# Optimization experiments

Hardware: AMD Instinct MI355X
Metric: run time of the kernel (lower is better)

Reference implementation:

```python
import jax, jax.numpy as jnp
import numpy as np

N = 33           # n_nodes (fixed by lstm1 input_size = 512*33)
T = 1024         # seq_length
E_RAND = 64      # random directed edges
E = E_RAND + N   # plus self-loops (PyG GATv2Conv add_self_loops=True)
H1, C1 = 8, 64   # gat1: heads, out_channels
C2 = 512         # gat2: out_channels, 1 head
D_IN, D_EDGE = 2, 3
HID1, HID2, N_CLASSES = 128, 64, 4


def _p(k, shape):
    return jax.random.normal(k, shape, dtype=jnp.float32) * 0.05


def setup_inputs() -> dict:
    key = jax.random.key(0)
    ks = jax.random.split(key, 30)
    src = jax.random.randint(ks[0], (E_RAND,), 0, N)
    dst = jax.random.randint(ks[1], (E_RAND,), 0, N)
    loop = jnp.arange(N)
    edge_index = jnp.stack([jnp.concatenate([src, loop]),
                            jnp.concatenate([dst, loop])]).astype(jnp.int32)
    return {
        'x': jax.random.normal(ks[2], (T, N, D_IN), dtype=jnp.float32),
        'edge_index': edge_index,
        'edge_attr': jax.random.normal(ks[3], (E, D_EDGE), dtype=jnp.float32),
        'g1_wl': _p(ks[4], (D_IN, H1 * C1)),
        'g1_wr': _p(ks[5], (D_IN, H1 * C1)),
        'g1_we': _p(ks[6], (D_EDGE, H1 * C1)),
        'g1_att': _p(ks[7], (H1, C1)),
        'g1_b': _p(ks[8], (H1 * C1,)),
        'g2_wl': _p(ks[9], (H1 * C1, C2)),
        'g2_wr': _p(ks[10], (H1 * C1, C2)),
        'g2_we': _p(ks[11], (D_EDGE, C2)),
        'g2_att': _p(ks[12], (1, C2)),
        'g2_b': _p(ks[13], (C2,)),
        'l1_wih': _p(ks[14], (4 * HID1, N * C2)),
        'l1_whh': _p(ks[15], (4 * HID1, HID1)),
        'l1_bih': _p(ks[16], (4 * HID1,)),
        'l1_bhh': _p(ks[17], (4 * HID1,)),
        'l2_wih': _p(ks[18], (4 * HID2, HID1)),
        'l2_whh': _p(ks[19], (4 * HID2, HID2)),
        'l2_bih': _p(ks[20], (4 * HID2,)),
        'l2_bhh': _p(ks[21], (4 * HID2,)),
        'fc_w': _p(ks[22], (N_CLASSES, HID2)),
        'fc_b': _p(ks[23], (N_CLASSES,)),
    }


def _gatv2(x, src, dst, edge_attr, wl, wr, we, att, bias, heads, ch):
    # GATv2 with edge features, vectorized over the time axis.
    # x: [T,N,Din] -> out [T,N,heads*ch]
    Tt, Nn, _ = x.shape
    xl = (x @ wl).reshape(Tt, Nn, heads, ch)   # source projection
    xr = (x @ wr).reshape(Tt, Nn, heads, ch)   # target projection
    ep = (edge_attr @ we).reshape(-1, heads, ch)
    msg = xl[:, src]                                        # [T,E,H,C]
    e = jax.nn.leaky_relu(msg + xr[:, dst] + ep[None], 0.2)  # GATv2 score input
    logits = jnp.einsum('tehc,hc->eth', e, att)             # edge-first [E,T,H]
    m = jax.ops.segment_max(logits, dst, num_segments=Nn)
    m = jnp.where(jnp.isneginf(m), 0.0, m)
    ex = jnp.exp(logits - m[dst])
    denom = jax.ops.segment_sum(ex, dst, num_segments=Nn)
    alpha = ex / (denom[dst] + 1e-16)                       # [E,T,H]
    out = jax.ops.segment_sum(alpha[..., None] * jnp.swapaxes(msg, 0, 1),
                              dst, num_segments=Nn)          # [N,T,H,C]
    return jnp.swapaxes(out, 0, 1).reshape(Tt, Nn, heads * ch) + bias


def _lstm(xs, wih, whh, bih, bhh):
    # PyTorch LSTM, batch=1, gate order i,f,g,o. xs: [T,D] -> [T,H]
    hd = whh.shape[1]
    def step(carry, xt):
        h, c = carry
        z = xt @ wih.T + h @ whh.T + bih + bhh
        i, f, g, o = jnp.split(z, 4)
        c = jax.nn.sigmoid(f) * c + jax.nn.sigmoid(i) * jnp.tanh(g)
        h = jax.nn.sigmoid(o) * jnp.tanh(c)
        return (h, c), h
    h0 = jnp.zeros((hd,), xs.dtype)
    _, hs = jax.lax.scan(step, (h0, h0), xs)
    return hs


def _forward(edge_index, x, edge_attr, g1_wl, g1_wr, g1_we, g1_att, g1_b,
             g2_wl, g2_wr, g2_we, g2_att, g2_b,
             l1_wih, l1_whh, l1_bih, l1_bhh,
             l2_wih, l2_whh, l2_bih, l2_bhh, fc_w, fc_b):
    src, dst = edge_index[0], edge_index[1]
    h = jax.nn.elu(_gatv2(x, src, dst, edge_attr, g1_wl, g1_wr, g1_we, g1_att, g1_b, H1, C1))
    h = jax.nn.elu(_gatv2(h, src, dst, edge_attr, g2_wl, g2_wr, g2_we, g2_att, g2_b, 1, C2))
    # torch: stack [T,N,512] -> permute(1,0,2) -> reshape(1, T, N*512)
    seq = jnp.transpose(h, (1, 0, 2)).reshape(T, N * C2)
    hs = _lstm(seq, l1_wih, l1_whh, l1_bih, l1_bhh)
    hs = _lstm(hs, l2_wih, l2_whh, l2_bih, l2_bhh)
    return (hs[-1] @ fc_w.T + fc_b)[None, :]  # [1, n_classes]


def reference(x, edge_index, edge_attr, g1_wl, g1_wr, g1_we, g1_att, g1_b,
              g2_wl, g2_wr, g2_we, g2_att, g2_b,
              l1_wih, l1_whh, l1_bih, l1_bhh,
              l2_wih, l2_whh, l2_bih, l2_bhh, fc_w, fc_b):
    return _forward(edge_index, x, edge_attr, g1_wl, g1_wr, g1_we, g1_att, g1_b,
                    g2_wl, g2_wr, g2_we, g2_att, g2_b,
                    l1_wih, l1_whh, l1_bih, l1_bhh,
                    l2_wih, l2_whh, l2_bih, l2_bhh, fc_w, fc_b)
```

## Files before the change

### kernel.cpp

```cpp
#include <hip/hip_runtime.h>

typedef unsigned short u16;
typedef unsigned int   u32;
typedef __attribute__((ext_vector_type(8))) short  short8;
typedef __attribute__((ext_vector_type(8))) unsigned short ushort8;
typedef __attribute__((ext_vector_type(4))) float  f32x4;

#define NT 1024
#define NN 33
#define NE 97

__device__ __forceinline__ float b2f(u16 u){ return __uint_as_float(((u32)u)<<16); }
__device__ __forceinline__ u16 f2b(float f){
    u32 x = __float_as_uint(f);
    return (u16)((x + 0x7fffu + ((x>>16)&1u)) >> 16);
}
__device__ __forceinline__ float sigm(float x){ return 1.f/(1.f+__expf(-x)); }
__device__ __forceinline__ float tanh_(float x){ float e=__expf(2.f*x); return 1.f - 2.f/(e+1.f); }

__global__ void detect_kernel(const u32* g1_wl_raw, int* flag){
    if (threadIdx.x==0 && blockIdx.x==0){
        int hits=0;
        for (int k=0;k<256;k++){
            u32 w = g1_wl_raw[k];
            u32 e = (w>>7)&0xffu;
            if (e>=96u && e<=126u) hits++;
        }
        *flag = (hits>=160) ? 0 : 1;
    }
}

struct ConvArgs { const void* src[22]; int n[22]; int off[22]; };
__global__ void convert_kernel(ConvArgs a, const int* flag, u16* blob){
    bool isf32 = (*flag)!=0;
    int stride = gridDim.x*blockDim.x;
    for (int s=0;s<22;s++){
        int n=a.n[s]; const void* sp=a.src[s]; u16* dp=blob+a.off[s];
        for (int i=blockIdx.x*blockDim.x+threadIdx.x; i<n; i+=stride)
            dp[i] = isf32 ? f2b(((const float*)sp)[i]) : ((const u16*)sp)[i];
    }
}

#define CX      0
#define CEA     67584
#define CG1WL   67880
#define CG1WR   68904
#define CG1WE   69928
#define CG1ATT  71464
#define CG1B    71976
#define CG2WL   72488
#define CG2WR   334632
#define CG2WE   596776
#define CG2ATT  598312
#define CG2B    598824
#define CL1WIH  599336
#define CL1WHH  9250088
#define CL1BIH  9315624
#define CL1BHH  9316136
#define CL2WIH  9316648
#define CL2WHH  9349416
#define CL2BIH  9365800
#define CL2BHH  9366056
#define CFCW    9366312
#define CFCB    9366568

__global__ void setup_kernel(const int* ei, const u16* ea,
                             const u16* g1_we, const u16* g2_we,
                             int* csr, float* ep1, float* ep2)
{
    int tid = threadIdx.x;
    if (tid == 0) {
        int cnt[NN]; for (int n=0;n<NN;n++) cnt[n]=0;
        for (int e=0;e<NE;e++) cnt[ei[NE+e]]++;
        int off=0;
        for (int n=0;n<NN;n++){ csr[n]=off; off+=cnt[n]; }
        csr[NN]=off;
        int pos[NN]; for (int n=0;n<NN;n++) pos[n]=csr[n];
        for (int e=0;e<NE;e++){ int d=ei[NE+e]; csr[34+pos[d]]=e; pos[d]++; }
        for (int e=0;e<NE;e++){ csr[131+e]=ei[e]; csr[228+e]=ei[NE+e]; }
    }
    for (int i=tid; i<NE*512; i+=blockDim.x) {
        int e = i>>9, hc = i&511;
        float a0=b2f(ea[e*3]), a1=b2f(ea[e*3+1]), a2=b2f(ea[e*3+2]);
        ep1[i] = a0*b2f(g1_we[hc]) + a1*b2f(g1_we[512+hc]) + a2*b2f(g1_we[1024+hc]);
        ep2[i] = a0*b2f(g2_we[hc]) + a1*b2f(g2_we[512+hc]) + a2*b2f(g2_we[1024+hc]);
    }
}

__global__ void wlrt_kernel(const u16* g2_wl, const u16* g2_wr, u16* wlrt)
{
    int i = blockIdx.x*256 + threadIdx.x;
    int k = i>>9, c = i&511;
    wlrt[c*512 + k]        = g2_wl[i];
    wlrt[(c+512)*512 + k]  = g2_wr[i];
}

__global__ __launch_bounds__(256) void gat1_kernel(
    const u16* x, const u16* g1_wl, const u16* g1_wr, const u16* g1_att,
    const u16* g1_b, const float* ep1, const int* csr, u16* h1)
{
    __shared__ float wl[2][512], wr[2][512], att[512], bias[512];
    __shared__ float xt[2*NN];
    __shared__ float logits[NE*8];
    __shared__ float mmax[NN*8], den[NN*8];
    __shared__ int s_off[NN+1], s_eid[NE], s_src[NE], s_dst[NE];
    int t = blockIdx.x, tid = threadIdx.x;

    for (int i=tid;i<512;i+=256){
        wl[0][i]=b2f(g1_wl[i]);      wl[1][i]=b2f(g1_wl[512+i]);
        wr[0][i]=b2f(g1_wr[i]);      wr[1][i]=b2f(g1_wr[512+i]);
        att[i]=b2f(g1_att[i]);       bias[i]=b2f(g1_b[i]);
    }
    for (int i=tid;i<2*NN;i+=256) xt[i]=b2f(x[t*(2*NN)+i]);
    if (tid<NN+1) s_off[tid]=csr[tid];
    for (int i=tid;i<NE;i+=256){ s_eid[i]=csr[34+i]; s_src[i]=csr[131+i]; s_dst[i]=csr[228+i]; }
    __syncthreads();

    for (int i=tid; i<NE*8; i+=256) {
        int e=i>>3, h=i&7;
        int s=s_src[e], d=s_dst[e];
        float xs0=xt[s*2], xs1=xt[s*2+1], xd0=xt[d*2], xd1=xt[d*2+1];
        const float* epp = ep1 + e*512 + h*64;
        float acc=0.f;
        #pragma unroll 8
        for (int c=0;c<64;c++){
            int hc=h*64+c;
            float v = xs0*wl[0][hc] + xs1*wl[1][hc]
                    + xd0*wr[0][hc] + xd1*wr[1][hc] + epp[c];
            v = v>0.f ? v : 0.2f*v;
            acc += att[hc]*v;
        }
        logits[i]=acc;
    }
    __syncthreads();
    for (int i=tid; i<NN*8; i+=256) {
        int n=i>>3, h=i&7;
        float m=-1e30f;
        for (int p=s_off[n]; p<s_off[n+1]; ++p){ float v=logits[s_eid[p]*8+h]; m=v>m?v:m; }
        float s=0.f;
        for (int p=s_off[n]; p<s_off[n+1]; ++p) s += __expf(logits[s_eid[p]*8+h]-m);
        mmax[i]=m; den[i]=s+1e-16f;
    }
    __syncthreads();
    for (int i=tid; i<NE*8; i+=256) {
        int h=i&7, d=s_dst[i>>3];
        logits[i] = __expf(logits[i]-mmax[d*8+h]) / den[d*8+h];
    }
    __syncthreads();
    for (int i=tid; i<NN*512; i+=256) {
        int n=i>>9, hc=i&511, h=hc>>6;
        float acc=0.f;
        for (int p=s_off[n]; p<s_off[n+1]; ++p){
            int e=s_eid[p]; int s=s_src[e];
            float xlv = xt[s*2]*wl[0][hc] + xt[s*2+1]*wl[1][hc];
            acc += logits[e*8+h]*xlv;
        }
        acc += bias[hc];
        acc = acc>0.f ? acc : __expf(acc)-1.f;
        h1[(size_t)(t*NN+n)*512 + hc] = f2b(acc);
    }
}

__global__ __launch_bounds__(256) void gemm_nt(
    const u16* __restrict__ A, const u16* __restrict__ B, void* Cout,
    int M, int N, int K, int kChunk, int mode)
{
    __shared__ u16 lds_a[128*40];
    __shared__ u16 lds_b[128*40];
    const int nt = blockIdx.x, mt = blockIdx.y, kc = blockIdx.z;
    const int tid = threadIdx.x;
    const int wave = tid>>6, lane = tid&63;
    const int wm = (wave&1)*64, wn = (wave>>1)*64;
    const int l15 = lane&15, quad = lane>>4;
    const int srow = tid>>2, scol = (tid&3)*8;

    const u16* Ab = A + (size_t)mt*128*K;
    const u16* Bb = B + (size_t)nt*128*K;
    const int k0beg = kc*kChunk, k0end = k0beg + kChunk;

    f32x4 acc[4][4] = {};
    for (int k0 = k0beg; k0 < k0end; k0 += 32) {
        #pragma unroll
        for (int r = 0; r < 2; ++r) {
            int row = srow + r*64;
            *(ushort8*)&lds_a[row*40 + scol] = *(const ushort8*)&Ab[(size_t)row*K + k0 + scol];
            *(ushort8*)&lds_b[row*40 + scol] = *(const ushort8*)&Bb[(size_t)row*K + k0 + scol];
        }
        __syncthreads();
        short8 af[4], bfr[4];
        #pragma unroll
        for (int i=0;i<4;i++) af[i]  = *(const short8*)&lds_a[(wm + i*16 + l15)*40 + quad*8];
        #pragma unroll
        for (int j=0;j<4;j++) bfr[j] = *(const short8*)&lds_b[(wn + j*16 + l15)*40 + quad*8];
        #pragma unroll
        for (int i=0;i<4;i++)
            #pragma unroll
            for (int j=0;j<4;j++)
                acc[i][j] = __builtin_amdgcn_mfma_f32_16x16x32_bf16(af[i], bfr[j], acc[i][j], 0,0,0);
        __syncthreads();
    }
    if (mode == 0) {
        u16* Cb = (u16*)Cout;
        #pragma unroll
        for (int i=0;i<4;i++)
            #pragma unroll
            for (int j=0;j<4;j++)
                #pragma unroll
                for (int r=0;r<4;r++){
                    int row = mt*128 + wm + i*16 + quad*4 + r;
                    int col = nt*128 + wn + j*16 + l15;
                    Cb[(size_t)row*N + col] = f2b(acc[i][j][r]);
                }
    } else {
        float* Cb = (float*)Cout + (size_t)kc*M*N;
        #pragma unroll
        for (int i=0;i<4;i++)
            #pragma unroll
            for (int j=0;j<4;j++)
                #pragma unroll
                for (int r=0;r<4;r++){
                    int row = mt*128 + wm + i*16 + quad*4 + r;
                    int col = nt*128 + wn + j*16 + l15;
                    Cb[(size_t)row*N + col] = acc[i][j][r];
                }
    }
}

__global__ void reduce8_kernel(const float* part, float* out)
{
    int i = blockIdx.x*256 + threadIdx.x;
    float s=0.f;
    #pragma unroll
    for (int k=0;k<8;k++) s += part[(size_t)k*524288 + i];
    out[i]=s;
}

__global__ __launch_bounds__(256) void gat2_kernel(
    const u16* C, const u16* g2_att, const u16* g2_b, const float* ep2,
    const int* csr, u16* h2)
{
    __shared__ u16 xl[NN*512];
    __shared__ float att[512], bias[512];
    __shared__ float part[NE*8];
    __shared__ float logit[NE], alpha[NE], mm[NN], dd[NN];
    __shared__ int s_off[NN+1], s_eid[NE], s_src[NE], s_dst[NE];
    int t = blockIdx.x, tid = threadIdx.x;

    for (int i=tid;i<512;i+=256){ att[i]=b2f(g2_att[i]); bias[i]=b2f(g2_b[i]); }
    if (tid<NN+1) s_off[tid]=csr[tid];
    for (int i=tid;i<NE;i+=256){ s_eid[i]=csr[34+i]; s_src[i]=csr[131+i]; s_dst[i]=csr[228+i]; }
    for (int i=tid; i<NN*64; i+=256){
        int n=i>>6, q=i&63;
        *(ushort8*)&xl[n*512+q*8] = *(const ushort8*)&C[(size_t)(t*NN+n)*1024 + q*8];
    }
    __syncthreads();

    for (int i=tid; i<NE*8; i+=256){
        int e=i>>3, q=i&7;
        int s=s_src[e], d=s_dst[e];
        const u16* xrp = C + (size_t)(t*NN+d)*1024 + 512 + q*64;
        const float* epp = ep2 + e*512 + q*64;
        const u16* xlp = xl + s*512 + q*64;
        float acc=0.f;
        #pragma unroll 8
        for (int c=0;c<64;c++){
            float v = b2f(xlp[c]) + b2f(xrp[c]) + epp[c];
            v = v>0.f ? v : 0.2f*v;
            acc += att[q*64+c]*v;
        }
        part[i]=acc;
    }
    __syncthreads();
    for (int i=tid;i<NE;i+=256){
        float s=0.f;
        #pragma unroll
        for (int q=0;q<8;q++) s+=part[i*8+q];
        logit[i]=s;
    }
    __syncthreads();
    for (int i=tid;i<NN;i+=256){
        float m=-1e30f;
        for (int p=s_off[i];p<s_off[i+1];++p){ float v=logit[s_eid[p]]; m=v>m?v:m; }
        float s=0.f;
        for (int p=s_off[i];p<s_off[i+1];++p) s+=__expf(logit[s_eid[p]]-m);
        mm[i]=m; dd[i]=s+1e-16f;
    }
    __syncthreads();
    for (int i=tid;i<NE;i+=256) alpha[i]=__expf(logit[i]-mm[s_dst[i]])/dd[s_dst[i]];
    __syncthreads();
    for (int i=tid;i<NN*512;i+=256){
        int n=i>>9, c=i&511;
        float acc=0.f;
        for (int p=s_off[n];p<s_off[n+1];++p){ int e=s_eid[p]; acc += alpha[e]*b2f(xl[s_src[e]*512+c]); }
        acc += bias[c];
        acc = acc>0.f ? acc : __expf(acc)-1.f;
        h2[(size_t)n*524288 + (size_t)t*512 + c] = f2b(acc);
    }
}

__global__ __launch_bounds__(512) void lstm_fused_kernel(
    const float* __restrict__ pre1,
    const u16* __restrict__ whh1, const u16* b1ih, const u16* b1hh,
    const u16* __restrict__ w2ih, const u16* __restrict__ w2hh,
    const u16* b2ih, const u16* b2hh,
    const u16* fc_w, const u16* fc_b, const int* flag, void* outv)
{
    __shared__ __align__(16) float pre_c[32*512];
    __shared__ __align__(16) u16 hb1[128];
    __shared__ __align__(16) u16 hb2[64];
    __shared__ __align__(16) float z_lds[768];
    __shared__ float hf[64];
    const int tid = threadIdx.x;
    const int wave = tid>>6, lane = tid&63;
    const int l15 = lane&15, quad = lane>>4;
    const bool keep = (l15==0);
    const short8 zer = {0,0,0,0,0,0,0,0};
    const f32x4 fz = {0.f,0.f,0.f,0.f};
    const float4* p4g = (const float4*)pre1;
    float4* c4 = (float4*)pre_c;

    if (tid<128) hb1[tid]=0;
    if (wave==7) hb2[lane]=0;

    if (wave < 4) {
        short8 af[8][4];
        #pragma unroll
        for (int i=0;i<8;i++)
            #pragma unroll
            for (int c=0;c<4;c++)
                af[i][c] = *(const short8*)&whh1[(size_t)(wave*128 + i*16 + l15)*128 + c*32 + quad*8];
        float bz0=0,bz1=0,bz2=0,bz3=0, c1=0.f;
        if (tid<128){
            bz0 = b2f(b1ih[tid])     + b2f(b1hh[tid]);
            bz1 = b2f(b1ih[128+tid]) + b2f(b1hh[128+tid]);
            bz2 = b2f(b1ih[256+tid]) + b2f(b1hh[256+tid]);
            bz3 = b2f(b1ih[384+tid]) + b2f(b1hh[384+tid]);
        }
        __syncthreads();
        for (int k=0;k<=1024;k++){
            if (k<1024 && (k&31)==0){
                #pragma unroll
                for (int j=0;j<8;j++) c4[j*512+tid] = p4g[(size_t)k*128 + j*512 + tid];
                __syncthreads();
            }
            short8 bf[4];
            #pragma unroll
            for (int c=0;c<4;c++){
                short8 v = *(const short8*)&hb1[c*32 + quad*8];
                bf[c] = keep ? v : zer;
            }
            #pragma unroll
            for (int i=0;i<8;i++){
                f32x4 a = __builtin_amdgcn_mfma_f32_16x16x32_bf16(af[i][0], bf[0], fz, 0,0,0);
                a = __builtin_amdgcn_mfma_f32_16x16x32_bf16(af[i][1], bf[1], a, 0,0,0);
                a = __builtin_amdgcn_mfma_f32_16x16x32_bf16(af[i][2], bf[2], a, 0,0,0);
                a = __builtin_amdgcn_mfma_f32_16x16x32_bf16(af[i][3], bf[3], a, 0,0,0);
                if (keep) *(f32x4*)&z_lds[wave*128 + i*16 + quad*4] = a;
            }
            __syncthreads();
            if (k<1024 && tid<128){
                const float* pc = pre_c + (k&31)*512;
                float zi=z_lds[tid]    +pc[tid]    +bz0;
                float zf=z_lds[128+tid]+pc[128+tid]+bz1;
                float zg=z_lds[256+tid]+pc[256+tid]+bz2;
                float zo=z_lds[384+tid]+pc[384+tid]+bz3;
                c1 = sigm(zf)*c1 + sigm(zi)*tanh_(zg);
                float ho = sigm(zo)*tanh_(c1);
                hb1[tid] = f2b(ho);
            }
            __syncthreads();
        }
    } else {
        const int wv = wave-4;
        short8 af[4][6];
        #pragma unroll
        for (int i=0;i<4;i++){
            int r = wv*64 + i*16 + l15;
            #pragma unroll
            for (int c=0;c<4;c++)
                af[i][c] = *(const short8*)&w2ih[(size_t)r*128 + c*32 + quad*8];
            #pragma unroll
            for (int c=0;c<2;c++)
                af[i][4+c] = *(const short8*)&w2hh[(size_t)r*64 + c*32 + quad*8];
        }
        float bz0=0,bz1=0,bz2=0,bz3=0, c2=0.f;
        if (wave==7){
            bz0 = b2f(b2ih[lane])     + b2f(b2hh[lane]);
            bz1 = b2f(b2ih[64+lane])  + b2f(b2hh[64+lane]);
            bz2 = b2f(b2ih[128+lane]) + b2f(b2hh[128+lane]);
            bz3 = b2f(b2ih[192+lane]) + b2f(b2hh[192+lane]);
        }
        __syncthreads();
        for (int k=0;k<=1024;k++){
            if (k<1024 && (k&31)==0){
                #pragma unroll
                for (int j=0;j<8;j++) c4[j*512+tid] = p4g[(size_t)k*128 + j*512 + tid];
                __syncthreads();
            }
            short8 bf[6];
            #pragma unroll
            for (int c=0;c<4;c++){
                short8 v = *(const short8*)&hb1[c*32 + quad*8];
                bf[c] = keep ? v : zer;
            }
            #pragma unroll
            for (int c=0;c<2;c++){
                short8 v = *(const short8*)&hb2[c*32 + quad*8];
                bf[4+c] = keep ? v : zer;
            }
            #pragma unroll
            for (int i=0;i<4;i++){
                f32x4 a = __builtin_amdgcn_mfma_f32_16x16x32_bf16(af[i][0], bf[0], fz, 0,0,0);
                a = __builtin_amdgcn_mfma_f32_16x16x32_bf16(af[i][1], bf[1], a, 0,0,0);
                a = __builtin_amdgcn_mfma_f32_16x16x32_bf16(af[i][2], bf[2], a, 0,0,0);
                a = __builtin_amdgcn_mfma_f32_16x16x32_bf16(af[i][3], bf[3], a, 0,0,0);
                a = __builtin_amdgcn_mfma_f32_16x16x32_bf16(af[i][4], bf[4], a, 0,0,0);
                a = __builtin_amdgcn_mfma_f32_16x16x32_bf16(af[i][5], bf[5], a, 0,0,0);
                if (keep) *(f32x4*)&z_lds[512 + wv*64 + i*16 + quad*4] = a;
            }
            __syncthreads();
            if (k>=1 && wave==7){
                float zi=z_lds[512+lane]+bz0, zf=z_lds[576+lane]+bz1;
                float zg=z_lds[640+lane]+bz2, zo=z_lds[704+lane]+bz3;
                c2 = sigm(zf)*c2 + sigm(zi)*tanh_(zg);
                float ho = sigm(zo)*tanh_(c2);
                hb2[lane] = f2b(ho);
                hf[lane] = ho;
            }
            __syncthreads();
        }
    }
    __syncthreads();
    if (tid<4){
        float acc = b2f(fc_b[tid]);
        #pragma unroll
        for (int j=0;j<64;j++) acc += hf[j]*b2f(fc_w[tid*64+j]);
        if (*flag) ((float*)outv)[tid] = acc;
        else       ((u16*)outv)[tid]  = f2b(acc);
    }
}

extern "C" void kernel_launch(void* const* d_in, const int* in_sizes, int n_in,
                              void* d_out, int out_size, void* d_ws, size_t ws_size,
                              hipStream_t stream) {
    const int* ei = (const int*)d_in[1];
    char* ws = (char*)d_ws;

    const size_t o_blob = 0;
    const size_t o_h    = 18733184;
    const size_t o_C    = o_h    + 34603008;
    const size_t o_wlrt = o_C    + 69206016;
    const size_t o_ep1  = o_wlrt + 1048576;
    const size_t o_ep2  = o_ep1  + 198656;
    const size_t o_csr  = o_ep2  + 198656;
    const size_t o_pre1 = o_csr  + 2048;

    u16*   blob  = (u16*)(ws + o_blob);
    u16*   h_buf = (u16*)(ws + o_h);
    u16*   Cbuf  = (u16*)(ws + o_C);
    u16*   wlrt  = (u16*)(ws + o_wlrt);
    float* ep1   = (float*)(ws + o_ep1);
    float* ep2   = (float*)(ws + o_ep2);
    int*   csr   = (int*)(ws + o_csr);
    int*   flag  = csr + 400;
    float* pre1  = (float*)(ws + o_pre1);
    float* part  = (float*)(ws + o_C);

    detect_kernel<<<1,64,0,stream>>>((const u32*)d_in[3], flag);

    ConvArgs ca;
    const int blob_off[22] = {CX,CEA,CG1WL,CG1WR,CG1WE,CG1ATT,CG1B,
                              CG2WL,CG2WR,CG2WE,CG2ATT,CG2B,
                              CL1WIH,CL1WHH,CL1BIH,CL1BHH,
                              CL2WIH,CL2WHH,CL2BIH,CL2BHH,CFCW,CFCB};
    const int in_idx[22]   = {0,2,3,4,5,6,7,8,9,10,11,12,13,14,15,16,17,18,19,20,21,22};
    for (int s=0;s<22;s++){
        ca.src[s]=d_in[in_idx[s]]; ca.n[s]=in_sizes[in_idx[s]]; ca.off[s]=blob_off[s];
    }
    convert_kernel<<<2048,256,0,stream>>>(ca, flag, blob);

    setup_kernel<<<1,256,0,stream>>>(ei, blob+CEA, blob+CG1WE, blob+CG2WE, csr, ep1, ep2);
    wlrt_kernel<<<1024,256,0,stream>>>(blob+CG2WL, blob+CG2WR, wlrt);
    gat1_kernel<<<NT,256,0,stream>>>(blob+CX, blob+CG1WL, blob+CG1WR, blob+CG1ATT,
                                     blob+CG1B, ep1, csr, h_buf);
    gemm_nt<<<dim3(8,264,1),256,0,stream>>>(h_buf, wlrt, Cbuf, 33792, 1024, 512, 512, 0);
    gat2_kernel<<<NT,256,0,stream>>>(Cbuf, blob+CG2ATT, blob+CG2B, ep2, csr, h_buf);
    gemm_nt<<<dim3(4,8,8),256,0,stream>>>(h_buf, blob+CL1WIH, part, 1024, 512, 16896, 2112, 1);
    reduce8_kernel<<<2048,256,0,stream>>>(part, pre1);
    lstm_fused_kernel<<<1,512,0,stream>>>(pre1,
        blob+CL1WHH, blob+CL1BIH, blob+CL1BHH,
        blob+CL2WIH, blob+CL2WHH, blob+CL2BIH, blob+CL2BHH,
        blob+CFCW, blob+CFCB, flag, d_out);
}
```

Baseline: 1.574 ms.

## Interleave LSTM gate rows so MFMA lanes compute cell updates in registers

A new kernel permutes the recurrent and input weight rows so the four gates of each hidden unit are adjacent, and the reduce kernel writes the precomputed input projections in the same interleaved order. Each MFMA lane therefore holds all four gate pre-activations for its unit and applies the LSTM cell update directly from registers. This removes the z_lds round-trip and one barrier per timestep. The hidden state is double-buffered in LDS so reads of the previous step and writes of the current step do not conflict. The cost is an extra small permute kernel and more complex lane-to-unit indexing.

```diff
diff --git a/kernel.cpp b/kernel.cpp
--- a/kernel.cpp
+++ b/kernel.cpp
@@ -95,6 +95,25 @@
     wlrt[(c+512)*512 + k]  = g2_wr[i];
 }
 
+__global__ void permw_kernel(const u16* w1hh, const u16* w2ih, const u16* w2hh,
+                             u16* w1p, u16* w2ip, u16* w2hp)
+{
+    int i0 = blockIdx.x*256 + threadIdx.x;
+    int stride = gridDim.x*256;
+    for (int j=i0; j<65536; j+=stride){
+        int r=j>>7, k=j&127, u=r>>2, g=r&3;
+        w1p[j] = w1hh[(g*128+u)*128 + k];
+    }
+    for (int j=i0; j<32768; j+=stride){
+        int r=j>>7, k=j&127, u=r>>2, g=r&3;
+        w2ip[j] = w2ih[(g*64+u)*128 + k];
+    }
+    for (int j=i0; j<16384; j+=stride){
+        int r=j>>6, k=j&63, u=r>>2, g=r&3;
+        w2hp[j] = w2hh[(g*64+u)*64 + k];
+    }
+}
+
 __global__ __launch_bounds__(256) void gat1_kernel(
     const u16* x, const u16* g1_wl, const u16* g1_wr, const u16* g1_att,
     const u16* g1_b, const float* ep1, const int* csr, u16* h1)
@@ -232,7 +251,8 @@
     float s=0.f;
     #pragma unroll
     for (int k=0;k<8;k++) s += part[(size_t)k*524288 + i];
-    out[i]=s;
+    int t=i>>9, c=i&511;
+    out[t*512 + ((c&127)<<2) + (c>>7)] = s;
 }
 
 __global__ __launch_bounds__(256) void gat2_kernel(
@@ -299,28 +319,25 @@
 }
 
 __global__ __launch_bounds__(512) void lstm_fused_kernel(
-    const float* __restrict__ pre1,
-    const u16* __restrict__ whh1, const u16* b1ih, const u16* b1hh,
-    const u16* __restrict__ w2ih, const u16* __restrict__ w2hh,
+    const float* __restrict__ pre1p,
+    const u16* __restrict__ w1p, const u16* b1ih, const u16* b1hh,
+    const u16* __restrict__ w2ip, const u16* __restrict__ w2hp,
     const u16* b2ih, const u16* b2hh,
     const u16* fc_w, const u16* fc_b, const int* flag, void* outv)
 {
     __shared__ __align__(16) float pre_c[32*512];
-    __shared__ __align__(16) u16 hb1[128];
-    __shared__ __align__(16) u16 hb2[64];
-    __shared__ __align__(16) float z_lds[768];
+    __shared__ __align__(16) u16 hb1[2][128];
+    __shared__ __align__(16) u16 hb2[2][64];
     __shared__ float hf[64];
     const int tid = threadIdx.x;
     const int wave = tid>>6, lane = tid&63;
     const int l15 = lane&15, quad = lane>>4;
-    const bool keep = (l15==0);
-    const short8 zer = {0,0,0,0,0,0,0,0};
     const f32x4 fz = {0.f,0.f,0.f,0.f};
-    const float4* p4g = (const float4*)pre1;
+    const float4* p4g = (const float4*)pre1p;
     float4* c4 = (float4*)pre_c;
 
-    if (tid<128) hb1[tid]=0;
-    if (wave==7) hb2[lane]=0;
+    if (tid<128) hb1[1][tid]=0;
+    if (tid<64)  hb2[1][tid]=0;
 
     if (wave < 4) {
         short8 af[8][4];
@@ -328,45 +345,49 @@
         for (int i=0;i<8;i++)
             #pragma unroll
             for (int c=0;c<4;c++)
-                af[i][c] = *(const short8*)&whh1[(size_t)(wave*128 + i*16 + l15)*128 + c*32 + quad*8];
-        float bz0=0,bz1=0,bz2=0,bz3=0, c1=0.f;
-        if (tid<128){
-            bz0 = b2f(b1ih[tid])     + b2f(b1hh[tid]);
-            bz1 = b2f(b1ih[128+tid]) + b2f(b1hh[128+tid]);
-            bz2 = b2f(b1ih[256+tid]) + b2f(b1hh[256+tid]);
-            bz3 = b2f(b1ih[384+tid]) + b2f(b1hh[384+tid]);
-        }
+                af[i][c] = *(const short8*)&w1p[(size_t)(wave*128 + i*16 + l15)*128 + c*32 + quad*8];
+        const int u = wave*32 + ((l15<8)?l15:0)*4 + quad;
+        const float bz0 = b2f(b1ih[u])     + b2f(b1hh[u]);
+        const float bz1 = b2f(b1ih[128+u]) + b2f(b1hh[128+u]);
+        const float bz2 = b2f(b1ih[256+u]) + b2f(b1hh[256+u]);
+        const float bz3 = b2f(b1ih[384+u]) + b2f(b1hh[384+u]);
+        float c1 = 0.f;
         __syncthreads();
-        for (int k=0;k<=1024;k++){
+        for (int k=0;k<1025;k++){
             if (k<1024 && (k&31)==0){
                 #pragma unroll
                 for (int j=0;j<8;j++) c4[j*512+tid] = p4g[(size_t)k*128 + j*512 + tid];
                 __syncthreads();
             }
-            short8 bf[4];
-            #pragma unroll
-            for (int c=0;c<4;c++){
-                short8 v = *(const short8*)&hb1[c*32 + quad*8];
-                bf[c] = keep ? v : zer;
-            }
-            #pragma unroll
-            for (int i=0;i<8;i++){
-                f32x4 a = __builtin_amdgcn_mfma_f32_16x16x32_bf16(af[i][0], bf[0], fz, 0,0,0);
-                a = __builtin_amdgcn_mfma_f32_16x16x32_bf16(af[i][1], bf[1], a, 0,0,0);
-                a = __builtin_amdgcn_mfma_f32_16x16x32_bf16(af[i][2], bf[2], a, 0,0,0);
-                a = __builtin_amdgcn_mfma_f32_16x16x32_bf16(af[i][3], bf[3], a, 0,0,0);
-                if (keep) *(f32x4*)&z_lds[wave*128 + i*16 + quad*4] = a;
-            }
-            __syncthreads();
-            if (k<1024 && tid<128){
-                const float* pc = pre_c + (k&31)*512;
-                float zi=z_lds[tid]    +pc[tid]    +bz0;
-                float zf=z_lds[128+tid]+pc[128+tid]+bz1;
-                float zg=z_lds[256+tid]+pc[256+tid]+bz2;
-                float zo=z_lds[384+tid]+pc[384+tid]+bz3;
-                c1 = sigm(zf)*c1 + sigm(zi)*tanh_(zg);
-                float ho = sigm(zo)*tanh_(c1);
-                hb1[tid] = f2b(ho);
+            if (k<1024){
+                float4 pf = {0.f,0.f,0.f,0.f};
+                if (l15<8) pf = *(const float4*)&pre_c[(k&31)*512 + wave*128 + l15*16 + quad*4];
+                const u16* hp = hb1[(k+1)&1];
+                short8 b0 = *(const short8*)&hp[quad*8];
+                short8 b1 = *(const short8*)&hp[32+quad*8];
+                short8 b2 = *(const short8*)&hp[64+quad*8];
+                short8 b3 = *(const short8*)&hp[96+quad*8];
+                f32x4 acc[8];
+                #pragma unroll
+                for (int i=0;i<8;i++){
+                    f32x4 a = __builtin_amdgcn_mfma_f32_16x16x32_bf16(af[i][0], b0, fz, 0,0,0);
+                    a = __builtin_amdgcn_mfma_f32_16x16x32_bf16(af[i][1], b1, a, 0,0,0);
+                    a = __builtin_amdgcn_mfma_f32_16x16x32_bf16(af[i][2], b2, a, 0,0,0);
+                    a = __builtin_amdgcn_mfma_f32_16x16x32_bf16(af[i][3], b3, a, 0,0,0);
+                    acc[i] = a;
+                }
+                f32x4 z = acc[0];
+                #pragma unroll
+                for (int i=1;i<8;i++) z = (l15==i) ? acc[i] : z;
+                if (l15<8){
+                    float zi = z[0]+pf.x+bz0;
+                    float zf = z[1]+pf.y+bz1;
+                    float zg = z[2]+pf.z+bz2;
+                    float zo = z[3]+pf.w+bz3;
+                    c1 = sigm(zf)*c1 + sigm(zi)*tanh_(zg);
+                    float ho = sigm(zo)*tanh_(c1);
+                    hb1[k&1][u] = f2b(ho);
+                }
             }
             __syncthreads();
         }
@@ -378,54 +399,57 @@
             int r = wv*64 + i*16 + l15;
             #pragma unroll
             for (int c=0;c<4;c++)
-                af[i][c] = *(const short8*)&w2ih[(size_t)r*128 + c*32 + quad*8];
+                af[i][c] = *(const short8*)&w2ip[(size_t)r*128 + c*32 + quad*8];
             #pragma unroll
             for (int c=0;c<2;c++)
-                af[i][4+c] = *(const short8*)&w2hh[(size_t)r*64 + c*32 + quad*8];
-        }
-        float bz0=0,bz1=0,bz2=0,bz3=0, c2=0.f;
-        if (wave==7){
-            bz0 = b2f(b2ih[lane])     + b2f(b2hh[lane]);
-            bz1 = b2f(b2ih[64+lane])  + b2f(b2hh[64+lane]);
-            bz2 = b2f(b2ih[128+lane]) + b2f(b2hh[128+lane]);
-            bz3 = b2f(b2ih[192+lane]) + b2f(b2hh[192+lane]);
-        }
+                af[i][4+c] = *(const short8*)&w2hp[(size_t)r*64 + c*32 + quad*8];
+        }
+        const int u2 = wv*16 + ((l15<4)?l15:0)*4 + quad;
+        const float bz0 = b2f(b2ih[u2])     + b2f(b2hh[u2]);
+        const float bz1 = b2f(b2ih[64+u2])  + b2f(b2hh[64+u2]);
+        const float bz2 = b2f(b2ih[128+u2]) + b2f(b2hh[128+u2]);
+        const float bz3 = b2f(b2ih[192+u2]) + b2f(b2hh[192+u2]);
+        float c2s = 0.f;
         __syncthreads();
-        for (int k=0;k<=1024;k++){
+        for (int k=0;k<1025;k++){
             if (k<1024 && (k&31)==0){
                 #pragma unroll
                 for (int j=0;j<8;j++) c4[j*512+tid] = p4g[(size_t)k*128 + j*512 + tid];
                 __syncthreads();
             }
-            short8 bf[6];
-            #pragma unroll
-            for (int c=0;c<4;c++){
-                short8 v = *(const short8*)&hb1[c*32 + quad*8];
-                bf[c] = keep ? v : zer;
-            }
-            #pragma unroll
-            for (int c=0;c<2;c++){
-                short8 v = *(const short8*)&hb2[c*32 + quad*8];
-                bf[4+c] = keep ? v : zer;
-            }
-            #pragma unroll
-            for (int i=0;i<4;i++){
-                f32x4 a = __builtin_amdgcn_mfma_f32_16x16x32_bf16(af[i][0], bf[0], fz, 0,0,0);
-                a = __builtin_amdgcn_mfma_f32_16x16x32_bf16(af[i][1], bf[1], a, 0,0,0);
-                a = __builtin_amdgcn_mfma_f32_16x16x32_bf16(af[i][2], bf[2], a, 0,0,0);
-                a = __builtin_amdgcn_mfma_f32_16x16x32_bf16(af[i][3], bf[3], a, 0,0,0);
-                a = __builtin_amdgcn_mfma_f32_16x16x32_bf16(af[i][4], bf[4], a, 0,0,0);
-                a = __builtin_amdgcn_mfma_f32_16x16x32_bf16(af[i][5], bf[5], a, 0,0,0);
-                if (keep) *(f32x4*)&z_lds[512 + wv*64 + i*16 + quad*4] = a;
-            }
-            __syncthreads();
-            if (k>=1 && wave==7){
-                float zi=z_lds[512+lane]+bz0, zf=z_lds[576+lane]+bz1;
-                float zg=z_lds[640+lane]+bz2, zo=z_lds[704+lane]+bz3;
-                c2 = sigm(zf)*c2 + sigm(zi)*tanh_(zg);
-                float ho = sigm(zo)*tanh_(c2);
-                hb2[lane] = f2b(ho);
-                hf[lane] = ho;
+            if (k>=1){
+                const u16* hp1 = hb1[(k-1)&1];
+                const u16* hp2 = hb2[k&1];
+                short8 b0 = *(const short8*)&hp1[quad*8];
+                short8 b1 = *(const short8*)&hp1[32+quad*8];
+                short8 b2 = *(const short8*)&hp1[64+quad*8];
+                short8 b3 = *(const short8*)&hp1[96+quad*8];
+                short8 b4 = *(const short8*)&hp2[quad*8];
+                short8 b5 = *(const short8*)&hp2[32+quad*8];
+                f32x4 acc[4];
+                #pragma unroll
+                for (int i=0;i<4;i++){
+                    f32x4 a = __builtin_amdgcn_mfma_f32_16x16x32_bf16(af[i][0], b0, fz, 0,0,0);
+                    a = __builtin_amdgcn_mfma_f32_16x16x32_bf16(af[i][1], b1, a, 0,0,0);
+                    a = __builtin_amdgcn_mfma_f32_16x16x32_bf16(af[i][2], b2, a, 0,0,0);
+                    a = __builtin_amdgcn_mfma_f32_16x16x32_bf16(af[i][3], b3, a, 0,0,0);
+                    a = __builtin_amdgcn_mfma_f32_16x16x32_bf16(af[i][4], b4, a, 0,0,0);
+                    a = __builtin_amdgcn_mfma_f32_16x16x32_bf16(af[i][5], b5, a, 0,0,0);
+                    acc[i] = a;
+                }
+                f32x4 z = acc[0];
+                #pragma unroll
+                for (int i=1;i<4;i++) z = (l15==i) ? acc[i] : z;
+                if (l15<4){
+                    float zi = z[0]+bz0;
+                    float zf = z[1]+bz1;
+                    float zg = z[2]+bz2;
+                    float zo = z[3]+bz3;
+                    c2s = sigm(zf)*c2s + sigm(zi)*tanh_(zg);
+                    float ho = sigm(zo)*tanh_(c2s);
+                    hb2[(k-1)&1][u2] = f2b(ho);
+                    hf[u2] = ho;
+                }
             }
             __syncthreads();
         }
@@ -454,6 +478,9 @@
     const size_t o_ep2  = o_ep1  + 198656;
     const size_t o_csr  = o_ep2  + 198656;
     const size_t o_pre1 = o_csr  + 2048;
+    const size_t o_w1p  = o_pre1 + 2097152;
+    const size_t o_w2ip = o_w1p  + 131072;
+    const size_t o_w2hp = o_w2ip + 65536;
 
     u16*   blob  = (u16*)(ws + o_blob);
     u16*   h_buf = (u16*)(ws + o_h);
@@ -464,6 +491,9 @@
     int*   csr   = (int*)(ws + o_csr);
     int*   flag  = csr + 400;
     float* pre1  = (float*)(ws + o_pre1);
+    u16*   w1p   = (u16*)(ws + o_w1p);
+    u16*   w2ip  = (u16*)(ws + o_w2ip);
+    u16*   w2hp  = (u16*)(ws + o_w2hp);
     float* part  = (float*)(ws + o_C);
 
     detect_kernel<<<1,64,0,stream>>>((const u32*)d_in[3], flag);
@@ -481,6 +511,7 @@
 
     setup_kernel<<<1,256,0,stream>>>(ei, blob+CEA, blob+CG1WE, blob+CG2WE, csr, ep1, ep2);
     wlrt_kernel<<<1024,256,0,stream>>>(blob+CG2WL, blob+CG2WR, wlrt);
+    permw_kernel<<<64,256,0,stream>>>(blob+CL1WHH, blob+CL2WIH, blob+CL2WHH, w1p, w2ip, w2hp);
     gat1_kernel<<<NT,256,0,stream>>>(blob+CX, blob+CG1WL, blob+CG1WR, blob+CG1ATT,
                                      blob+CG1B, ep1, csr, h_buf);
     gemm_nt<<<dim3(8,264,1),256,0,stream>>>(h_buf, wlrt, Cbuf, 33792, 1024, 512, 512, 0);
@@ -488,7 +519,7 @@
     gemm_nt<<<dim3(4,8,8),256,0,stream>>>(h_buf, blob+CL1WIH, part, 1024, 512, 16896, 2112, 1);
     reduce8_kernel<<<2048,256,0,stream>>>(part, pre1);
     lstm_fused_kernel<<<1,512,0,stream>>>(pre1,
-        blob+CL1WHH, blob+CL1BIH, blob+CL1BHH,
-        blob+CL2WIH, blob+CL2WHH, blob+CL2BIH, blob+CL2BHH,
+        w1p, blob+CL1BIH, blob+CL1BHH,
+        w2ip, w2hp, blob+CL2BIH, blob+CL2BHH,
         blob+CFCW, blob+CFCB, flag, d_out);
 }
```

Measured after the change: 1.502 ms. 4.6% less time.
